# Optimization experiments

Measured on AMD Instinct MI355X. Metric: run time of the kernel, lower is better.

## Reference

```python
import math
import jax, jax.numpy as jnp
import numpy as np

B, W, L, E, ORD = 4, 768, 8192, 33, 64


def setup_inputs() -> dict:
    key = jax.random.key(0)
    ks = jax.random.split(key, 8)
    x = jax.random.normal(ks[0], (B, W, L), jnp.float32)
    # PositionalEmbedding z: [1, L, E] = [time, Re(exp(-i f w)), Im(exp(-i f w))]
    bands = (E - 1) // 2
    time_emb = jnp.linspace(0.0, 1.0, L)[None, :, None]
    t_resc = jnp.linspace(0.0, L - 1, L)[None, :, None]
    w_ang = 2.0 * math.pi * t_resc / L
    f = jnp.linspace(1e-4, bands - 1, bands)[None, None]
    zc = jnp.exp(-1j * f * w_ang)
    z = jnp.concatenate([time_emb, zc.real, zc.imag], axis=-1).astype(jnp.float32)
    # Sin activation frequency (shared across all activations)
    freq = jnp.ones((1, ORD), jnp.float32)
    # implicit filter MLP weights
    s_in, s_h = 1.0 / math.sqrt(E), 1.0 / math.sqrt(ORD)
    w0 = jax.random.normal(ks[1], (E, ORD), jnp.float32) * s_in
    b0 = jnp.zeros((ORD,), jnp.float32)
    w1 = jax.random.normal(ks[2], (ORD, ORD), jnp.float32) * s_h
    b1 = jnp.zeros((ORD,), jnp.float32)
    w2 = jax.random.normal(ks[3], (ORD, ORD), jnp.float32) * s_h
    b2 = jnp.zeros((ORD,), jnp.float32)
    wf = jax.random.normal(ks[4], (ORD, W), jnp.float32) * s_h  # no bias
    # ExponentialModulation deltas: [1, 1, W]
    max_decay = math.log(0.01) / 0.3
    min_decay = math.log(0.01) / 1.5
    deltas = jnp.linspace(min_decay, max_decay, W)[None, None].astype(jnp.float32)
    # residual bias D ~ normal init
    D = jax.random.normal(ks[5], (W,), jnp.float32) * 0.01
    return dict(x=x, z=z, freq=freq, w0=w0, b0=b0, w1=w1, b1=b1,
                w2=w2, b2=b2, wf=wf, deltas=deltas, D=D)


def reference(x, z, freq, w0, b0, w1, b1, w2, b2, wf, deltas, D):
    seq_len = x.shape[-1]
    fft_size = 2 * seq_len
    # implicit filter MLP: z [1, L, E] -> h [1, L, W]
    h = jnp.sin(freq * (z @ w0 + b0))
    h = jnp.sin(freq * (h @ w1 + b1))
    h = jnp.sin(freq * (h @ w2 + b2))
    h = h @ wf
    # exponential modulation (shift = 0)
    t = jnp.linspace(0.0, 1.0, seq_len)[None, :, None]  # [1, L, 1]
    h = h * jnp.exp(-t * jnp.abs(deltas))
    k = h[0].T  # [W, L]
    # FFT long convolution
    k_f = jnp.fft.rfft(k, n=fft_size) / fft_size        # [W, L+1] complex
    u_f = jnp.fft.rfft(x, n=fft_size)                   # [B, W, L+1] complex
    y = jnp.fft.irfft(u_f * k_f, n=fft_size, norm='forward')[..., :seq_len]
    return (y + x * D[:, None]).astype(x.dtype)
```

## Files before the change

### kernel.cpp

```cpp
#include <hip/hip_runtime.h>

#define BSZ   4
#define WSEQ  768
#define LSEQ  8192
#define NFFT  8192
#define MH    4096
#define EMB   33
#define ORDER 64

#define KFROW   16448
#define WS_TWN  0
#define WS_TW2N 4096
#define WS_H    20480
#define WS_KF   544768

__device__ __forceinline__ int swz(int a){ return a ^ (((a >> 5) & 7) << 2); }

__global__ void tables_kernel(float* __restrict__ ws){
  int t = blockIdx.x * 256 + threadIdx.x;
  const double TWO_PI = 6.283185307179586476925286766559;
  if (t < 2048){
    double ang = -TWO_PI * (double)t / 8192.0;
    ws[WS_TWN + 2*t]   = (float)cos(ang);
    ws[WS_TWN + 2*t+1] = (float)sin(ang);
  }
  int k = t - 2048;
  if (k >= 0 && k < NFFT){
    double ang = -TWO_PI * (double)k / 16384.0;
    ws[WS_TW2N + 2*k]   = (float)cos(ang);
    ws[WS_TW2N + 2*k+1] = (float)sin(ang);
  }
}

__global__ void mlp_kernel(const float* __restrict__ z, const float* __restrict__ freq,
                           const float* __restrict__ w0, const float* __restrict__ b0,
                           const float* __restrict__ w1, const float* __restrict__ b1,
                           const float* __restrict__ w2, const float* __restrict__ b2,
                           float* __restrict__ ws){
  int l = blockIdx.x * 256 + threadIdx.x;
  if (l >= LSEQ) return;
  float zv[EMB];
  #pragma unroll
  for (int e = 0; e < EMB; ++e) zv[e] = z[l*EMB + e];
  float h1[ORDER];
  #pragma unroll 2
  for (int o = 0; o < ORDER; ++o){
    float a = b0[o];
    #pragma unroll
    for (int e = 0; e < EMB; ++e) a += zv[e] * w0[e*ORDER + o];
    h1[o] = sinf(freq[o] * a);
  }
  float h2[ORDER];
  #pragma unroll 2
  for (int o = 0; o < ORDER; ++o){
    float a = b1[o];
    #pragma unroll
    for (int p = 0; p < ORDER; ++p) a += h1[p] * w1[p*ORDER + o];
    h2[o] = sinf(freq[o] * a);
  }
  #pragma unroll 2
  for (int o = 0; o < ORDER; ++o){
    float a = b2[o];
    #pragma unroll
    for (int p = 0; p < ORDER; ++p) a += h2[p] * w2[p*ORDER + o];
    ws[WS_H + o*LSEQ + l] = sinf(freq[o] * a);
  }
}

__global__ void __launch_bounds__(256, 2)
kgemm_kernel(const float* __restrict__ wf, const float* __restrict__ deltas,
             float* __restrict__ ws){
  __shared__ float As[64][128];
  __shared__ float Bs[64][128];
  const int tid = threadIdx.x;
  const int lb = (blockIdx.x & 63) << 7;
  const int wb = (blockIdx.x >> 6) << 7;
  #pragma unroll
  for (int q = 0; q < 8; ++q){
    int idx = q*256 + tid;
    int o = idx >> 5;
    int c = (idx & 31) << 2;
    *(float4*)&As[o][c] = *(const float4*)&ws[WS_H + o*LSEQ + lb + c];
    *(float4*)&Bs[o][c] = *(const float4*)&wf[o*WSEQ + wb + c];
  }
  __syncthreads();
  const int tx = tid & 15;
  const int ty = tid >> 4;
  float acc[8][8];
  #pragma unroll
  for (int i = 0; i < 8; ++i)
    #pragma unroll
    for (int j = 0; j < 8; ++j) acc[i][j] = 0.f;
  #pragma unroll 4
  for (int ko = 0; ko < 64; ++ko){
    float a[8], b[8];
    #pragma unroll
    for (int i = 0; i < 8; ++i) a[i] = As[ko][ty*8 + i];
    #pragma unroll
    for (int j = 0; j < 8; ++j) b[j] = Bs[ko][tx + j*16];
    #pragma unroll
    for (int i = 0; i < 8; ++i)
      #pragma unroll
      for (int j = 0; j < 8; ++j) acc[i][j] += a[i]*b[j];
  }
  const float ool = 1.0f / 8191.0f;
  #pragma unroll
  for (int j = 0; j < 8; ++j){
    int w = wb + tx + j*16;
    float ad = fabsf(deltas[w]);
    float e[8];
    #pragma unroll
    for (int i = 0; i < 8; ++i){
      float tl = (float)(lb + ty*8 + i) * ool;
      e[i] = acc[i][j] * __expf(-tl * ad);
    }
    float* dst = ws + WS_KF + (size_t)w*KFROW + lb + ty*8;
    *(float4*)dst       = make_float4(e[0], e[1], e[2], e[3]);
    *(float4*)(dst + 4) = make_float4(e[4], e[5], e[6], e[7]);
  }
}

__device__ __forceinline__ void pass_r4(float2* sC,
        const float2* __restrict__ twN, int tid, int l2, float sgn){
  int ns = 1 << l2;
  int sh = 11 - l2;
  float2 o[8][4];
  int bas[8];
  #pragma unroll
  for (int i = 0; i < 8; ++i){
    int j = tid + (i << 8);
    int u = j & (ns - 1);
    float2 t = twN[u << sh];
    float w1r = t.x,               w1i = sgn * t.y;
    float w2r = w1r*w1r - w1i*w1i, w2i = 2.f*w1r*w1i;
    float w3r = w2r*w1r - w2i*w1i, w3i = w2r*w1i + w2i*w1r;
    float2 v0 = sC[swz(j)];
    float2 a1 = sC[swz(j+2048)];
    float2 a2 = sC[swz(j+4096)];
    float2 a3 = sC[swz(j+6144)];
    float v1r = a1.x*w1r - a1.y*w1i, v1i = a1.x*w1i + a1.y*w1r;
    float v2r = a2.x*w2r - a2.y*w2i, v2i = a2.x*w2i + a2.y*w2r;
    float v3r = a3.x*w3r - a3.y*w3i, v3i = a3.x*w3i + a3.y*w3r;
    float t0r = v0.x+v2r, t0i = v0.y+v2i;
    float t1r = v0.x-v2r, t1i = v0.y-v2i;
    float t2r = v1r+v3r, t2i = v1i+v3i;
    float t3r = v1r-v3r, t3i = v1i-v3i;
    o[i][0] = make_float2(t0r+t2r,       t0i+t2i);
    o[i][2] = make_float2(t0r-t2r,       t0i-t2i);
    o[i][1] = make_float2(t1r + sgn*t3i, t1i - sgn*t3r);
    o[i][3] = make_float2(t1r - sgn*t3i, t1i + sgn*t3r);
    bas[i] = ((j >> l2) << (l2 + 2)) + u;
  }
  __syncthreads();
  #pragma unroll
  for (int i = 0; i < 8; ++i){
    #pragma unroll
    for (int r = 0; r < 4; ++r){
      sC[swz(bas[i] + (r << l2))] = o[i][r];
    }
  }
  __syncthreads();
}

__device__ __forceinline__ void fft_passes(float2* sC,
        const float2* __restrict__ twN, int tid, float sgn){
  #pragma unroll 1
  for (int p = 0; p < 6; ++p)
    pass_r4(sC, twN, tid, 1 + 2*p, sgn);
}

__device__ __forceinline__ void pass_r2_first(float2* sC, int tid){
  float4 v[16];
  #pragma unroll
  for (int i = 0; i < 16; ++i){
    int j = tid + (i << 8);
    float2 a = sC[swz(j)];
    float2 b = sC[swz(j+4096)];
    v[i] = make_float4(a.x+b.x, a.y+b.y, a.x-b.x, a.y-b.y);
  }
  __syncthreads();
  #pragma unroll
  for (int i = 0; i < 16; ++i){
    int j = tid + (i << 8);
    ((float4*)sC)[swz(2*j) >> 1] = v[i];
  }
  __syncthreads();
}

__device__ __forceinline__ void unpack_item(int t, const float2* sC,
        const float2* __restrict__ tw2N,
        float& Ukr, float& Uki, float& Unr, float& Uni){
  int tn = (NFFT - t) & (NFFT - 1);
  float2 a = sC[swz(t)];
  float2 b = sC[swz(tn)];
  float Er = 0.5f*(a.x+b.x), Ei = 0.5f*(a.y-b.y);
  float Pr = 0.5f*(a.x-b.x), Pi = 0.5f*(a.y+b.y);
  float Or = Pi, Oi = -Pr;
  float2 tw = tw2N[t];
  float Qr = Or*tw.x - Oi*tw.y, Qi = Or*tw.y + Oi*tw.x;
  Ukr = Er + Qr; Uki = Ei + Qi;
  Unr = Er - Qr; Uni = Qi - Ei;
}

__global__ void __launch_bounds__(256, 2)
fftk_kernel(float* __restrict__ ws){
  __shared__ float2 sC[NFFT];
  const int tid = threadIdx.x;
  const int w = blockIdx.x;
  float* kfr = ws + WS_KF + (size_t)w * KFROW;
  const float2* twN  = (const float2*)(ws + WS_TWN);
  const float2* tw2N = (const float2*)(ws + WS_TW2N);
  #pragma unroll
  for (int q = 0; q < 16; ++q){
    int j = tid + (q << 8);
    float2 v = ((const float2*)kfr)[j];
    ((float4*)sC)[swz(2*j) >> 1] = make_float4(v.x, v.y, v.x, v.y);
  }
  __syncthreads();
  fft_passes(sC, twN, tid, 1.0f);
  const float sc = 1.0f / 16384.0f;
  #pragma unroll
  for (int i = 0; i < 16; ++i){
    int t = tid + (i << 8);
    float Ukr, Uki, Unr, Uni;
    unpack_item(t, sC, tw2N, Ukr, Uki, Unr, Uni);
    ((float2*)kfr)[t]        = make_float2(Ukr*sc, Uki*sc);
    ((float2*)kfr)[NFFT - t] = make_float2(Unr*sc, Uni*sc);
  }
  if (tid == 0){
    float Ukr, Uki, Unr, Uni;
    unpack_item(MH, sC, tw2N, Ukr, Uki, Unr, Uni);
    ((float2*)kfr)[MH] = make_float2(Ukr*sc, Uki*sc);
  }
}

__device__ __forceinline__ void pair_item(int t, const float2* sC,
        const float* __restrict__ kfr, const float2* __restrict__ tw2N,
        float& Dtr, float& Dti, float& Dnr, float& Dni){
  float Ukr, Uki, Unr, Uni;
  unpack_item(t, sC, tw2N, Ukr, Uki, Unr, Uni);
  float2 tw = tw2N[t];
  float2 Kk = ((const float2*)kfr)[t];
  float2 Kn = ((const float2*)kfr)[NFFT - t];
  float Ykr = Ukr*Kk.x - Uki*Kk.y, Yki = Ukr*Kk.y + Uki*Kk.x;
  float Ynr = Unr*Kn.x - Uni*Kn.y, Yni = Unr*Kn.y + Uni*Kn.x;
  float Ar = Ykr + Ynr, Ai = Yki - Yni;
  float Br = Ykr - Ynr, Bi = Yki + Yni;
  float Rr = Br*tw.x + Bi*tw.y;
  float Ri = Bi*tw.x - Br*tw.y;
  Dtr = Ar - Ri; Dti = Ai + Rr;
  Dnr = Ar + Ri; Dni = Rr - Ai;
}

__global__ void __launch_bounds__(256, 2)
conv_kernel(const float* __restrict__ x, const float* __restrict__ ws,
            const float* __restrict__ Dw, float* __restrict__ out){
  __shared__ float2 sC[NFFT];
  const int tid = threadIdx.x;
  const int blk = (blockIdx.x & 7) * 384 + (blockIdx.x >> 3);
  const int b = blk & 3, w = blk >> 2;
  const float2* twN  = (const float2*)(ws + WS_TWN);
  const float2* tw2N = (const float2*)(ws + WS_TW2N);
  const float* kfr = ws + WS_KF + (size_t)w * KFROW;
  const size_t rowoff = ((size_t)(b*WSEQ + w)) * LSEQ;
  const float2* xrow = (const float2*)(x + rowoff);
  float2 xr[16];
  #pragma unroll
  for (int q = 0; q < 16; ++q){
    int j = tid + (q << 8);
    float2 v = xrow[j];
    xr[q] = v;
    ((float4*)sC)[swz(2*j) >> 1] = make_float4(v.x, v.y, v.x, v.y);
  }
  __syncthreads();
  fft_passes(sC, twN, tid, 1.0f);
  float2 Dt[16], Dn[16];
  float etr = 0.f, eti = 0.f;
  #pragma unroll
  for (int i = 0; i < 16; ++i){
    int t = tid + (i << 8);
    float a, bq, c, d;
    pair_item(t, sC, kfr, tw2N, a, bq, c, d);
    Dt[i] = make_float2(a, bq); Dn[i] = make_float2(c, d);
  }
  if (tid == 0){
    float a, bq, c, d;
    pair_item(MH, sC, kfr, tw2N, a, bq, c, d);
    etr = a; eti = bq;
  }
  __syncthreads();
  #pragma unroll
  for (int i = 0; i < 16; ++i){
    int t = tid + (i << 8);
    int tn = (NFFT - t) & (NFFT - 1);
    sC[swz(t)]  = Dt[i];
    sC[swz(tn)] = Dn[i];
  }
  if (tid == 0){ sC[swz(MH)] = make_float2(etr, eti); }
  __syncthreads();
  pass_r2_first(sC, tid);
  fft_passes(sC, twN, tid, -1.0f);
  const float dsc = Dw[w];
  float2* orow = (float2*)(out + rowoff);
  #pragma unroll
  for (int q = 0; q < 16; ++q){
    int j = tid + (q << 8);
    float2 dv = sC[swz(j)];
    float2 o;
    o.x = dv.x + xr[q].x * dsc;
    o.y = dv.y + xr[q].y * dsc;
    orow[j] = o;
  }
}

extern "C" void kernel_launch(void* const* d_in, const int* in_sizes, int n_in,
                              void* d_out, int out_size, void* d_ws, size_t ws_size,
                              hipStream_t stream){
  const float* x      = (const float*)d_in[0];
  const float* z      = (const float*)d_in[1];
  const float* freq   = (const float*)d_in[2];
  const float* w0     = (const float*)d_in[3];
  const float* b0     = (const float*)d_in[4];
  const float* w1     = (const float*)d_in[5];
  const float* b1     = (const float*)d_in[6];
  const float* w2     = (const float*)d_in[7];
  const float* b2     = (const float*)d_in[8];
  const float* wf     = (const float*)d_in[9];
  const float* deltas = (const float*)d_in[10];
  const float* Dw     = (const float*)d_in[11];
  float* ws  = (float*)d_ws;
  float* out = (float*)d_out;

  tables_kernel<<<dim3(40),  dim3(256), 0, stream>>>(ws);
  mlp_kernel   <<<dim3(32),  dim3(256), 0, stream>>>(z, freq, w0, b0, w1, b1, w2, b2, ws);
  kgemm_kernel <<<dim3(384), dim3(256), 0, stream>>>(wf, deltas, ws);
  fftk_kernel  <<<dim3(WSEQ), dim3(256), 0, stream>>>(ws);
  conv_kernel  <<<dim3(BSZ*WSEQ), dim3(256), 0, stream>>>(x, ws, Dw, out);
}
```

Before: 557.8 us.

## Use 512-thread FFT blocks with full twiddle tables and templated sign

Doubles the threads per block for the FFT and conv kernels to 512, so each thread handles half as many butterflies and keeps fewer registers live. It also enlarges the twiddle table so w2 and w3 are loaded directly rather than computed by complex multiplies, and turns the FFT direction sign into a template parameter. The aim is higher occupancy and less ALU work per pass, in exchange for more table loads and a changed workspace layout.

Result: slower. 712.1 us (+27.7%).

```diff
diff --git a/kernel.cpp b/kernel.cpp
--- a/kernel.cpp
+++ b/kernel.cpp
@@ -7,29 +7,25 @@
 #define MH    4096
 #define EMB   33
 #define ORDER 64
-
-#define KFROW   16448
+#define NT    512
+
+#define KFROW   16392
 #define WS_TWN  0
-#define WS_TW2N 4096
-#define WS_H    20480
-#define WS_KF   544768
+#define WS_TW2N 16384
+#define WS_H    32768
+#define WS_KF   557056
 
 __device__ __forceinline__ int swz(int a){ return a ^ (((a >> 5) & 7) << 2); }
 
 __global__ void tables_kernel(float* __restrict__ ws){
   int t = blockIdx.x * 256 + threadIdx.x;
   const double TWO_PI = 6.283185307179586476925286766559;
-  if (t < 2048){
-    double ang = -TWO_PI * (double)t / 8192.0;
-    ws[WS_TWN + 2*t]   = (float)cos(ang);
-    ws[WS_TWN + 2*t+1] = (float)sin(ang);
-  }
-  int k = t - 2048;
-  if (k >= 0 && k < NFFT){
-    double ang = -TWO_PI * (double)k / 16384.0;
-    ws[WS_TW2N + 2*k]   = (float)cos(ang);
-    ws[WS_TW2N + 2*k+1] = (float)sin(ang);
-  }
+  double a1 = -TWO_PI * (double)t / 8192.0;
+  double a2 = -TWO_PI * (double)t / 16384.0;
+  ws[WS_TWN  + 2*t]   = (float)cos(a1);
+  ws[WS_TWN  + 2*t+1] = (float)sin(a1);
+  ws[WS_TW2N + 2*t]   = (float)cos(a2);
+  ws[WS_TW2N + 2*t+1] = (float)sin(a2);
 }
 
 __global__ void mlp_kernel(const float* __restrict__ z, const float* __restrict__ freq,
@@ -120,20 +116,24 @@
   }
 }
 
+template<int SGN>
 __device__ __forceinline__ void pass_r4(float2* sC,
-        const float2* __restrict__ twN, int tid, int l2, float sgn){
-  int ns = 1 << l2;
-  int sh = 11 - l2;
-  float2 o[8][4];
-  int bas[8];
-  #pragma unroll
-  for (int i = 0; i < 8; ++i){
-    int j = tid + (i << 8);
+        const float2* __restrict__ twN, int tid, int l2){
+  const int ns = 1 << l2;
+  const int sh = 11 - l2;
+  float2 o[4][4];
+  int bas[4];
+  #pragma unroll
+  for (int i = 0; i < 4; ++i){
+    int j = tid + (i << 9);
     int u = j & (ns - 1);
-    float2 t = twN[u << sh];
-    float w1r = t.x,               w1i = sgn * t.y;
-    float w2r = w1r*w1r - w1i*w1i, w2i = 2.f*w1r*w1i;
-    float w3r = w2r*w1r - w2i*w1i, w3i = w2r*w1i + w2i*w1r;
+    int i1 = u << sh;
+    float2 t1 = twN[i1];
+    float2 t2 = twN[2*i1];
+    float2 t3 = twN[3*i1];
+    float w1r = t1.x, w1i = (SGN > 0) ? t1.y : -t1.y;
+    float w2r = t2.x, w2i = (SGN > 0) ? t2.y : -t2.y;
+    float w3r = t3.x, w3i = (SGN > 0) ? t3.y : -t3.y;
     float2 v0 = sC[swz(j)];
     float2 a1 = sC[swz(j+2048)];
     float2 a2 = sC[swz(j+4096)];
@@ -142,18 +142,23 @@
     float v2r = a2.x*w2r - a2.y*w2i, v2i = a2.x*w2i + a2.y*w2r;
     float v3r = a3.x*w3r - a3.y*w3i, v3i = a3.x*w3i + a3.y*w3r;
     float t0r = v0.x+v2r, t0i = v0.y+v2i;
-    float t1r = v0.x-v2r, t1i = v0.y-v2i;
+    float t1r_ = v0.x-v2r, t1i_ = v0.y-v2i;
     float t2r = v1r+v3r, t2i = v1i+v3i;
     float t3r = v1r-v3r, t3i = v1i-v3i;
-    o[i][0] = make_float2(t0r+t2r,       t0i+t2i);
-    o[i][2] = make_float2(t0r-t2r,       t0i-t2i);
-    o[i][1] = make_float2(t1r + sgn*t3i, t1i - sgn*t3r);
-    o[i][3] = make_float2(t1r - sgn*t3i, t1i + sgn*t3r);
+    o[i][0] = make_float2(t0r+t2r, t0i+t2i);
+    o[i][2] = make_float2(t0r-t2r, t0i-t2i);
+    if (SGN > 0){
+      o[i][1] = make_float2(t1r_ + t3i, t1i_ - t3r);
+      o[i][3] = make_float2(t1r_ - t3i, t1i_ + t3r);
+    } else {
+      o[i][1] = make_float2(t1r_ - t3i, t1i_ + t3r);
+      o[i][3] = make_float2(t1r_ + t3i, t1i_ - t3r);
+    }
     bas[i] = ((j >> l2) << (l2 + 2)) + u;
   }
   __syncthreads();
   #pragma unroll
-  for (int i = 0; i < 8; ++i){
+  for (int i = 0; i < 4; ++i){
     #pragma unroll
     for (int r = 0; r < 4; ++r){
       sC[swz(bas[i] + (r << l2))] = o[i][r];
@@ -162,26 +167,27 @@
   __syncthreads();
 }
 
+template<int SGN>
 __device__ __forceinline__ void fft_passes(float2* sC,
-        const float2* __restrict__ twN, int tid, float sgn){
+        const float2* __restrict__ twN, int tid){
   #pragma unroll 1
   for (int p = 0; p < 6; ++p)
-    pass_r4(sC, twN, tid, 1 + 2*p, sgn);
+    pass_r4<SGN>(sC, twN, tid, 1 + 2*p);
 }
 
 __device__ __forceinline__ void pass_r2_first(float2* sC, int tid){
-  float4 v[16];
-  #pragma unroll
-  for (int i = 0; i < 16; ++i){
-    int j = tid + (i << 8);
+  float4 v[8];
+  #pragma unroll
+  for (int i = 0; i < 8; ++i){
+    int j = tid + (i << 9);
     float2 a = sC[swz(j)];
     float2 b = sC[swz(j+4096)];
     v[i] = make_float4(a.x+b.x, a.y+b.y, a.x-b.x, a.y-b.y);
   }
   __syncthreads();
   #pragma unroll
-  for (int i = 0; i < 16; ++i){
-    int j = tid + (i << 8);
+  for (int i = 0; i < 8; ++i){
+    int j = tid + (i << 9);
     ((float4*)sC)[swz(2*j) >> 1] = v[i];
   }
   __syncthreads();
@@ -202,7 +208,7 @@
   Unr = Er - Qr; Uni = Qi - Ei;
 }
 
-__global__ void __launch_bounds__(256, 2)
+__global__ void __launch_bounds__(NT, 4)
 fftk_kernel(float* __restrict__ ws){
   __shared__ float2 sC[NFFT];
   const int tid = threadIdx.x;
@@ -211,17 +217,17 @@
   const float2* twN  = (const float2*)(ws + WS_TWN);
   const float2* tw2N = (const float2*)(ws + WS_TW2N);
   #pragma unroll
-  for (int q = 0; q < 16; ++q){
-    int j = tid + (q << 8);
+  for (int q = 0; q < 8; ++q){
+    int j = tid + (q << 9);
     float2 v = ((const float2*)kfr)[j];
     ((float4*)sC)[swz(2*j) >> 1] = make_float4(v.x, v.y, v.x, v.y);
   }
   __syncthreads();
-  fft_passes(sC, twN, tid, 1.0f);
+  fft_passes<1>(sC, twN, tid);
   const float sc = 1.0f / 16384.0f;
   #pragma unroll
-  for (int i = 0; i < 16; ++i){
-    int t = tid + (i << 8);
+  for (int i = 0; i < 8; ++i){
+    int t = tid + (i << 9);
     float Ukr, Uki, Unr, Uni;
     unpack_item(t, sC, tw2N, Ukr, Uki, Unr, Uni);
     ((float2*)kfr)[t]        = make_float2(Ukr*sc, Uki*sc);
@@ -252,7 +258,7 @@
   Dnr = Ar + Ri; Dni = Rr - Ai;
 }
 
-__global__ void __launch_bounds__(256, 2)
+__global__ void __launch_bounds__(NT, 4)
 conv_kernel(const float* __restrict__ x, const float* __restrict__ ws,
             const float* __restrict__ Dw, float* __restrict__ out){
   __shared__ float2 sC[NFFT];
@@ -264,21 +270,21 @@
   const float* kfr = ws + WS_KF + (size_t)w * KFROW;
   const size_t rowoff = ((size_t)(b*WSEQ + w)) * LSEQ;
   const float2* xrow = (const float2*)(x + rowoff);
-  float2 xr[16];
-  #pragma unroll
-  for (int q = 0; q < 16; ++q){
-    int j = tid + (q << 8);
+  float2 xr[8];
+  #pragma unroll
+  for (int q = 0; q < 8; ++q){
+    int j = tid + (q << 9);
     float2 v = xrow[j];
     xr[q] = v;
     ((float4*)sC)[swz(2*j) >> 1] = make_float4(v.x, v.y, v.x, v.y);
   }
   __syncthreads();
-  fft_passes(sC, twN, tid, 1.0f);
-  float2 Dt[16], Dn[16];
+  fft_passes<1>(sC, twN, tid);
+  float2 Dt[8], Dn[8];
   float etr = 0.f, eti = 0.f;
   #pragma unroll
-  for (int i = 0; i < 16; ++i){
-    int t = tid + (i << 8);
+  for (int i = 0; i < 8; ++i){
+    int t = tid + (i << 9);
     float a, bq, c, d;
     pair_item(t, sC, kfr, tw2N, a, bq, c, d);
     Dt[i] = make_float2(a, bq); Dn[i] = make_float2(c, d);
@@ -290,8 +296,8 @@
   }
   __syncthreads();
   #pragma unroll
-  for (int i = 0; i < 16; ++i){
-    int t = tid + (i << 8);
+  for (int i = 0; i < 8; ++i){
+    int t = tid + (i << 9);
     int tn = (NFFT - t) & (NFFT - 1);
     sC[swz(t)]  = Dt[i];
     sC[swz(tn)] = Dn[i];
@@ -299,12 +305,12 @@
   if (tid == 0){ sC[swz(MH)] = make_float2(etr, eti); }
   __syncthreads();
   pass_r2_first(sC, tid);
-  fft_passes(sC, twN, tid, -1.0f);
+  fft_passes<-1>(sC, twN, tid);
   const float dsc = Dw[w];
   float2* orow = (float2*)(out + rowoff);
   #pragma unroll
-  for (int q = 0; q < 16; ++q){
-    int j = tid + (q << 8);
+  for (int q = 0; q < 8; ++q){
+    int j = tid + (q << 9);
     float2 dv = sC[swz(j)];
     float2 o;
     o.x = dv.x + xr[q].x * dsc;
@@ -331,9 +337,9 @@
   float* ws  = (float*)d_ws;
   float* out = (float*)d_out;
 
-  tables_kernel<<<dim3(40),  dim3(256), 0, stream>>>(ws);
+  tables_kernel<<<dim3(32),  dim3(256), 0, stream>>>(ws);
   mlp_kernel   <<<dim3(32),  dim3(256), 0, stream>>>(z, freq, w0, b0, w1, b1, w2, b2, ws);
   kgemm_kernel <<<dim3(384), dim3(256), 0, stream>>>(wf, deltas, ws);
-  fftk_kernel  <<<dim3(WSEQ), dim3(256), 0, stream>>>(ws);
-  conv_kernel  <<<dim3(BSZ*WSEQ), dim3(256), 0, stream>>>(x, ws, Dw, out);
-}
+  fftk_kernel  <<<dim3(WSEQ), dim3(NT), 0, stream>>>(ws);
+  conv_kernel  <<<dim3(BSZ*WSEQ), dim3(NT), 0, stream>>>(x, ws, Dw, out);
+}
```
